# Performance work log

Hardware: AMD Instinct MI355X
Metric: run time of the kernel (lower is better)

Reference implementation:

```python
import jax, jax.numpy as jnp
import numpy as np

N_KNN = 16
BN_EPS = 1e-5


def conv1d(x, w, b):
    # x: [B, Cin, N], w: [Cout, Cin], b: [Cout] (1x1 Conv1d)
    return jnp.einsum('oc,bcn->bon', w, x) + b[None, :, None]


def conv2d(x, w, b):
    # x: [B, Cin, N, K], w: [Cout, Cin], b: [Cout] (1x1 Conv2d)
    return jnp.einsum('oc,bcnk->bonk', w, x) + b[None, :, None, None]


def bn2d(x, gamma, beta, mean, var):
    # eval-mode BatchNorm2d over channel axis 1
    scale = (gamma / jnp.sqrt(var + BN_EPS))[None, :, None, None]
    return (x - mean[None, :, None, None]) * scale + beta[None, :, None, None]


def knn_idx(pos, k):
    # pos: [B, 3, N] -> idx: [B, N, K] of k nearest neighbors (incl. self)
    p = jnp.swapaxes(pos, 1, 2)  # [B, N, 3]
    sq = jnp.sum(p * p, axis=-1)  # [B, N]
    d2 = sq[:, :, None] - 2.0 * jnp.einsum('bnd,bmd->bnm', p, p) + sq[:, None, :]
    _, idx = jax.lax.top_k(-d2, k)
    return idx


def group(x, idx):
    # x: [B, C, N], idx: [B, N, K] -> [B, C, N, K] (grouping_operation)
    return jax.vmap(lambda xb, ib: xb[:, ib])(x, idx)


def setup_inputs() -> dict:
    key = jax.random.key(0)
    B, C_OBJ, C_Q, N, DIM, PH, AM = 4, 512, 512, 4096, 128, 64, 4
    ks = jax.random.split(key, 32)
    r = lambda i, sh, s=0.05: jax.random.normal(ks[i], sh, jnp.float32) * s
    inp = {
        'obj_feature': jax.random.normal(ks[0], (B, C_OBJ, N), jnp.float32),
        'pos': jax.random.normal(ks[1], (B, 3, N), jnp.float32),
        'query_points': jax.random.normal(ks[2], (B, C_Q, N), jnp.float32),
        # linear_start_query / linear_start_obj
        'w_sq': r(3, (DIM, C_Q)), 'b_sq': r(4, (DIM,)),
        'w_so': r(5, (DIM, C_OBJ)), 'b_so': r(6, (DIM,)),
        # key / query / value 1x1 convs
        'w_k': r(7, (DIM, DIM)), 'b_k': r(8, (DIM,)),
        'w_q': r(9, (DIM, DIM)), 'b_q': r(10, (DIM,)),
        'w_v': r(11, (DIM, DIM)), 'b_v': r(12, (DIM,)),
        # pos_mlp: Conv2d(3->PH), BN, ReLU, Conv2d(PH->DIM)
        'w_p1': r(13, (PH, 3)), 'b_p1': r(14, (PH,)),
        'g_bn1': 1.0 + r(15, (PH,)), 'be_bn1': r(16, (PH,)),
        'm_bn1': r(17, (PH,)), 'v_bn1': 1.0 + 0.1 * jax.random.uniform(ks[18], (PH,), jnp.float32),
        'w_p2': r(19, (DIM, PH)), 'b_p2': r(20, (DIM,)),
        # attn_mlp: Conv2d(DIM->DIM*AM), BN, ReLU, Conv2d(DIM*AM->DIM)
        'w_a1': r(21, (DIM * AM, DIM)), 'b_a1': r(22, (DIM * AM,)),
        'g_bn2': 1.0 + r(23, (DIM * AM,)), 'be_bn2': r(24, (DIM * AM,)),
        'm_bn2': r(25, (DIM * AM,)), 'v_bn2': 1.0 + 0.1 * jax.random.uniform(ks[26], (DIM * AM,), jnp.float32),
        # linear_end
        'w_e': r(27, (C_OBJ, DIM)), 'b_e': r(28, (C_OBJ,)),
    }
    return inp


def reference(obj_feature, pos, query_points, w_sq, b_sq, w_so, b_so, w_k, b_k,
              w_q, b_q, w_v, b_v, w_p1, b_p1, g_bn1, be_bn1, m_bn1, v_bn1,
              w_p2, b_p2, w_a1, b_a1, g_bn2, be_bn2, m_bn2, v_bn2, w_e, b_e):
    qf = conv1d(query_points, w_sq, b_sq)          # [B, dim, N]
    f = conv1d(obj_feature, w_so, b_so)            # [B, dim, N]
    idx = knn_idx(jax.lax.stop_gradient(pos), N_KNN)  # [B, N, K]
    key_g = group(conv1d(f, w_k, b_k), idx)        # [B, dim, N, K]
    value = conv1d(f, w_v, b_v)                    # [B, dim, N]
    query = conv1d(qf, w_q, b_q)                   # [B, dim, N]
    qk_rel = query[:, :, :, None] - key_g          # [B, dim, N, K]
    pos_rel = pos[:, :, :, None] - group(pos, idx)  # [B, 3, N, K]
    pe = conv2d(jax.nn.relu(bn2d(conv2d(pos_rel, w_p1, b_p1), g_bn1, be_bn1, m_bn1, v_bn1)), w_p2, b_p2)
    attn = conv2d(jax.nn.relu(bn2d(conv2d(qk_rel + pe, w_a1, b_a1), g_bn2, be_bn2, m_bn2, v_bn2)), w_a2_placeholder := w_p2 * 0 + 0, b_p2 * 0) if False else None
    hidden = jax.nn.relu(bn2d(conv2d(qk_rel + pe, w_a1, b_a1), g_bn2, be_bn2, m_bn2, v_bn2))
    attn = jax.nn.softmax(conv2d(hidden, w_a2, b_a2), axis=-1)  # softmax over K
    v = value[:, :, :, None] + pe                  # [B, dim, N, K]
    agg = jnp.sum(attn * v, axis=-1)               # 'b c i j, b c i j -> b c i'
    return conv1d(agg, w_e, b_e)                   # [B, C_obj, N]

# fix: w_a2/b_a2 are parameters; re-declare reference cleanly to include them

def _setup_extra(inp):
    kk = jax.random.split(jax.random.key(7), 2)
    inp['w_a2'] = jax.random.normal(kk[0], (128, 512), jnp.float32) * 0.05
    inp['b_a2'] = jax.random.normal(kk[1], (128,), jnp.float32) * 0.05
    return inp

_orig_setup = setup_inputs

def setup_inputs():
    return _setup_extra(_orig_setup())


def reference(obj_feature, pos, query_points, w_sq, b_sq, w_so, b_so, w_k, b_k,
              w_q, b_q, w_v, b_v, w_p1, b_p1, g_bn1, be_bn1, m_bn1, v_bn1,
              w_p2, b_p2, w_a1, b_a1, g_bn2, be_bn2, m_bn2, v_bn2, w_a2, b_a2,
              w_e, b_e):
    qf = conv1d(query_points, w_sq, b_sq)
    f = conv1d(obj_feature, w_so, b_so)
    idx = knn_idx(jax.lax.stop_gradient(pos), N_KNN)
    key_g = group(conv1d(f, w_k, b_k), idx)
    value = conv1d(f, w_v, b_v)
    query = conv1d(qf, w_q, b_q)
    qk_rel = query[:, :, :, None] - key_g
    pos_rel = pos[:, :, :, None] - group(pos, idx)
    pe = conv2d(jax.nn.relu(bn2d(conv2d(pos_rel, w_p1, b_p1), g_bn1, be_bn1, m_bn1, v_bn1)), w_p2, b_p2)
    hidden = jax.nn.relu(bn2d(conv2d(qk_rel + pe, w_a1, b_a1), g_bn2, be_bn2, m_bn2, v_bn2))
    attn = jax.nn.softmax(conv2d(hidden, w_a2, b_a2), axis=-1)
    v = value[:, :, :, None] + pe
    agg = jnp.sum(attn * v, axis=-1)
    return conv1d(agg, w_e, b_e)
```

## Files before the change

### kernel.cpp

```cpp
#include <hip/hip_runtime.h>

typedef __bf16 bf16;
typedef __bf16 bf16x8 __attribute__((ext_vector_type(8)));
typedef __bf16 bf16x4 __attribute__((ext_vector_type(4)));
typedef __bf16 bf16x2 __attribute__((ext_vector_type(2)));
typedef float f32x4 __attribute__((ext_vector_type(4)));

#define MFMA16(a,b,c) __builtin_amdgcn_mfma_f32_16x16x32_bf16((a),(b),(c),0,0,0)

#define NPTS 4096
#define CIN 512
#define DIM 128
#define PH 64
#define HID 512

#define OFF_WQS 0u
#define OFF_WKO (128u*1024u)
#define OFF_WVO (256u*1024u)
#define OFF_BQS (384u*1024u)
#define OFF_BKO (385u*1024u)
#define OFF_BVO (386u*1024u)
#define OFF_S1  (387u*1024u)
#define OFF_T1  (388u*1024u)
#define OFF_S2  (389u*1024u)
#define OFF_T2  (391u*1024u)
#define OFF_CW  (400u*1024u)
#define OFF_QT  (1u<<20)
#define OFF_KT  (OFF_QT + (4u<<20))
#define OFF_VT  (OFF_QT + (8u<<20))
#define OFF_IDX (OFF_QT + (12u<<20))
#define WS_NEED (OFF_QT + (13u<<20))

struct P {
  const float* in[31];
  char* ws;
  float* out;
  int ybase;
};

template<int C> __device__ __forceinline__ float rorf(float x){
  return __int_as_float(__builtin_amdgcn_mov_dpp(__float_as_int(x), 0x120|C, 0xF, 0xF, true));
}
__device__ __forceinline__ float red16max(float x){
  x=fmaxf(x,rorf<1>(x)); x=fmaxf(x,rorf<2>(x)); x=fmaxf(x,rorf<4>(x)); x=fmaxf(x,rorf<8>(x)); return x;
}
__device__ __forceinline__ float red16sum(float x){
  x+=rorf<1>(x); x+=rorf<2>(x); x+=rorf<4>(x); x+=rorf<8>(x); return x;
}
template<int C> __device__ __forceinline__ unsigned long long ror64(unsigned long long k){
  unsigned lo = (unsigned)__builtin_amdgcn_mov_dpp((int)(unsigned)k,        0x120|C, 0xF, 0xF, true);
  unsigned hi = (unsigned)__builtin_amdgcn_mov_dpp((int)(unsigned)(k>>32), 0x120|C, 0xF, 0xF, true);
  return ((unsigned long long)hi<<32)|lo;
}

__global__ __launch_bounds__(256) void k_fold(P p) {
  int tid = blockIdx.x*256 + threadIdx.x;
  char* ws = p.ws;
  if (tid < 196608) {
    int m_id = tid >> 16, o = (tid >> 9) & 127, c = tid & 511;
    const float* A  = m_id==0 ? p.in[9] : (m_id==1 ? p.in[7] : p.in[11]);
    const float* Bm = (m_id==0) ? p.in[3] : p.in[5];
    float acc = 0.f;
    #pragma unroll 8
    for (int m=0;m<128;m++) acc += A[o*128+m] * Bm[m*512+c];
    bf16* outw = (bf16*)(ws + (m_id==0?OFF_WQS: m_id==1?OFF_WKO:OFF_WVO));
    outw[o*512+c] = (bf16)acc;
  } else if (tid < 196992) {
    int t = tid - 196608; int m_id = t >> 7, o = t & 127;
    const float* A  = m_id==0 ? p.in[9] : (m_id==1 ? p.in[7] : p.in[11]);
    const float* bb = (m_id==0) ? p.in[4] : p.in[6];
    const float* bs = m_id==0 ? p.in[10] : (m_id==1 ? p.in[8] : p.in[12]);
    float acc = bs[o];
    for (int m=0;m<128;m++) acc += A[o*128+m] * bb[m];
    float* ob = (float*)(ws + (m_id==0?OFF_BQS: m_id==1?OFF_BKO:OFF_BVO));
    ob[o] = acc;
  } else if (tid < 197056) {
    int i = tid - 196992;
    float s = p.in[15][i] * rsqrtf(p.in[18][i] + 1e-5f);
    ((float*)(ws+OFF_S1))[i] = s;
    ((float*)(ws+OFF_T1))[i] = (p.in[14][i] - p.in[17][i])*s + p.in[16][i];
  } else if (tid < 197568) {
    int i = tid - 197056;
    float s = p.in[23][i] * rsqrtf(p.in[26][i] + 1e-5f);
    ((float*)(ws+OFF_S2))[i] = s;
    ((float*)(ws+OFF_T2))[i] = (p.in[22][i] - p.in[25][i])*s + p.in[24][i];
  } else if (tid < 223168) {
    int e0 = (tid - 197568) * 8;
    const float* src; int base;
    if (e0 < 8192)        { src = p.in[19]; base = 0; }
    else if (e0 < 73728)  { src = p.in[21]; base = 8192; }
    else if (e0 < 139264) { src = p.in[29]; base = 73728; }
    else                  { src = p.in[27]; base = 139264; }
    const float* sp = src + (e0 - base);
    f32x4 a = *(const f32x4*)sp, b2 = *(const f32x4*)(sp+4);
    bf16x8 o8;
    o8[0]=(bf16)a[0]; o8[1]=(bf16)a[1]; o8[2]=(bf16)a[2]; o8[3]=(bf16)a[3];
    o8[4]=(bf16)b2[0]; o8[5]=(bf16)b2[1]; o8[6]=(bf16)b2[2]; o8[7]=(bf16)b2[3];
    *(bf16x8*)((bf16*)(ws+OFF_CW) + e0) = o8;
  }
}

__global__ __launch_bounds__(256) void k_knn(P p) {
  int lane = threadIdx.x & 63, w = threadIdx.x >> 6;
  int ig = blockIdx.x*4 + w;
  int b = ig >> 12, n = ig & 4095;
  const float* pb = p.in[1] + b*3*NPTS;
  float qx = pb[n], qy = pb[NPTS+n], qz = pb[2*NPTS+n];
  float sqn = __fadd_rn(__fadd_rn(__fmul_rn(qx,qx), __fmul_rn(qy,qy)), __fmul_rn(qz,qz));
  unsigned u[64];
  #pragma unroll
  for (int t=0;t<64;t++) {
    int j = t*64 + lane;
    float xj=pb[j], yj=pb[NPTS+j], zj=pb[2*NPTS+j];
    float sqj = __fadd_rn(__fadd_rn(__fmul_rn(xj,xj), __fmul_rn(yj,yj)), __fmul_rn(zj,zj));
    float dot = __fadd_rn(__fadd_rn(__fmul_rn(qx,xj), __fmul_rn(qy,yj)), __fmul_rn(qz,zj));
    float d2 = __fadd_rn(__fsub_rn(sqn, __fmul_rn(2.f,dot)), sqj);
    unsigned bb2 = __float_as_uint(d2);
    u[t] = bb2 ^ (((unsigned)((int)bb2 >> 31)) | 0x80000000u);
  }
  int* op = (int*)(p.ws + OFF_IDX) + ig*16;
  int tsel_s = 64; bool mine = false;
  #pragma unroll 1
  for (int r=0;r<16;r++) {
    switch (tsel_s) {
#define CLR(T) case T: u[T] = mine ? 0xFFFFFFFFu : u[T]; break;
      CLR(0) CLR(1) CLR(2) CLR(3) CLR(4) CLR(5) CLR(6) CLR(7)
      CLR(8) CLR(9) CLR(10) CLR(11) CLR(12) CLR(13) CLR(14) CLR(15)
      CLR(16) CLR(17) CLR(18) CLR(19) CLR(20) CLR(21) CLR(22) CLR(23)
      CLR(24) CLR(25) CLR(26) CLR(27) CLR(28) CLR(29) CLR(30) CLR(31)
      CLR(32) CLR(33) CLR(34) CLR(35) CLR(36) CLR(37) CLR(38) CLR(39)
      CLR(40) CLR(41) CLR(42) CLR(43) CLR(44) CLR(45) CLR(46) CLR(47)
      CLR(48) CLR(49) CLR(50) CLR(51) CLR(52) CLR(53) CLR(54) CLR(55)
      CLR(56) CLR(57) CLR(58) CLR(59) CLR(60) CLR(61) CLR(62) CLR(63)
#undef CLR
      default: break;
    }
    unsigned v0=u[0], v1=u[16], v2=u[32], v3=u[48];
    int t0=0, t1=16, t2=32, t3=48;
    #pragma unroll
    for (int i=1;i<16;i++) {
      { bool lt=u[i]    <v0; v0=lt?u[i]   :v0; t0=lt?(i)   :t0; }
      { bool lt=u[16+i] <v1; v1=lt?u[16+i]:v1; t1=lt?(16+i):t1; }
      { bool lt=u[32+i] <v2; v2=lt?u[32+i]:v2; t2=lt?(32+i):t2; }
      { bool lt=u[48+i] <v3; v3=lt?u[48+i]:v3; t3=lt?(48+i):t3; }
    }
    { bool lt=v1<v0; v0=lt?v1:v0; t0=lt?t1:t0; }
    { bool lt=v3<v2; v2=lt?v3:v2; t2=lt?t3:t2; }
    { bool lt=v2<v0; v0=lt?v2:v0; t0=lt?t2:t0; }
    unsigned long long key = ((unsigned long long)v0 << 12) | (unsigned)((t0<<6) | lane);
    { unsigned long long o = ror64<1>(key); if (o<key) key=o; }
    { unsigned long long o = ror64<2>(key); if (o<key) key=o; }
    { unsigned long long o = ror64<4>(key); if (o<key) key=o; }
    { unsigned long long o = ror64<8>(key); if (o<key) key=o; }
    { unsigned long long o = __shfl_xor(key,16); if (o<key) key=o; }
    { unsigned long long o = __shfl_xor(key,32); if (o<key) key=o; }
    unsigned jwin = (unsigned)key & 4095u;
    if (lane==0) op[r] = (int)jwin;
    tsel_s = __builtin_amdgcn_readfirstlane((int)(jwin>>6));
    mine = ((int)(jwin&63)==lane);
  }
}

__global__ __launch_bounds__(256) void k_qkv(P p) {
  int mat = blockIdx.z, b = blockIdx.y, n0 = blockIdx.x*64;
  int tid = threadIdx.x, lane = tid&63, w = tid>>6;
  const float* in = (mat==0 ? p.in[2] : p.in[0]) + b*CIN*NPTS;
  const bf16* W = (const bf16*)(p.ws + (mat==0?OFF_WQS: mat==1?OFF_WKO:OFF_WVO));
  const float* bias = (const float*)(p.ws + (mat==0?OFF_BQS: mat==1?OFF_BKO:OFF_BVO));
  bf16* outT = (bf16*)(p.ws + (mat==0?OFF_QT: mat==1?OFF_KT:OFF_VT)) + (b*NPTS + n0)*DIM;
  __shared__ __align__(16) bf16 Bl[64*40];
  f32x4 acc[8] = {};
  for (int ks=0; ks<16; ks++) {
    int c0 = ks*32;
    {
      int cc = tid>>3, nn0 = (tid&7)*8;
      const float* sp = in + (c0+cc)*NPTS + n0 + nn0;
      f32x4 a = *(const f32x4*)sp, b2 = *(const f32x4*)(sp+4);
      Bl[(nn0+0)*40+cc]=(bf16)a[0];  Bl[(nn0+1)*40+cc]=(bf16)a[1];
      Bl[(nn0+2)*40+cc]=(bf16)a[2];  Bl[(nn0+3)*40+cc]=(bf16)a[3];
      Bl[(nn0+4)*40+cc]=(bf16)b2[0]; Bl[(nn0+5)*40+cc]=(bf16)b2[1];
      Bl[(nn0+6)*40+cc]=(bf16)b2[2]; Bl[(nn0+7)*40+cc]=(bf16)b2[3];
    }
    __syncthreads();
    int ncol = w*16 + (lane&15);
    bf16x8 bfr = *(const bf16x8*)(&Bl[ncol*40 + (lane>>4)*8]);
    #pragma unroll
    for (int ot=0;ot<8;ot++) {
      bf16x8 af = *(const bf16x8*)(W + (ot*16 + (lane&15))*CIN + c0 + (lane>>4)*8);
      acc[ot] = MFMA16(af, bfr, acc[ot]);
    }
    __syncthreads();
  }
  int o0 = (lane>>4)*4;
  int nloc = w*16 + (lane&15);
  #pragma unroll
  for (int ot=0;ot<8;ot++) {
    f32x4 bs = *(const f32x4*)(bias + ot*16 + o0);
    bf16x4 st;
    st[0]=(bf16)(acc[ot][0]+bs[0]); st[1]=(bf16)(acc[ot][1]+bs[1]);
    st[2]=(bf16)(acc[ot][2]+bs[2]); st[3]=(bf16)(acc[ot][3]+bs[3]);
    *(bf16x4*)(outT + nloc*DIM + ot*16 + o0) = st;
  }
}

__global__ __launch_bounds__(512) void k_fused(P p) {
  int bb = p.ybase + blockIdx.y, pt0 = blockIdx.x*8;
  int tid=threadIdx.x, lane=tid&63, w=tid>>6;
  int c = lane&15, g = lane>>4;
  char* ws = p.ws;
  const bf16* qT = (const bf16*)(ws+OFF_QT) + bb*NPTS*DIM;
  const bf16* kT = (const bf16*)(ws+OFF_KT) + bb*NPTS*DIM;
  const bf16* vT = (const bf16*)(ws+OFF_VT) + bb*NPTS*DIM;
  const int* idxg = (const int*)(ws+OFF_IDX) + (bb*NPTS + pt0)*16;
  const bf16* wp2b = (const bf16*)(ws+OFF_CW);
  const bf16* wa1b = wp2b + 8192;
  const bf16* wa2b = wa1b + 65536;
  const bf16* web  = wa2b + 65536;
  const float* s2 = (const float*)(ws+OFF_S2);
  const float* t2 = (const float*)(ws+OFF_T2);
  __shared__ __align__(16) char LB[53248];
  bf16* Xl = (bf16*)LB;
  bf16* HT = (bf16*)(LB + 34816);
  bf16* aggl = (bf16*)(LB + 34816);

  {
    int col = w*16 + c;
    int j = idxg[col] & 4095;
    const float* pb = p.in[1] + bb*3*NPTS;
    int n = pt0 + w;
    float r0 = pb[n]-pb[j], r1 = pb[NPTS+n]-pb[NPTS+j], r2 = pb[2*NPTS+n]-pb[2*NPTS+j];
    const float* wp1 = p.in[13];
    const float* s1 = (const float*)(ws+OFF_S1);
    const float* t1 = (const float*)(ws+OFF_T1);
    #pragma unroll
    for (int i=0;i<16;i+=2) {
      int m = g*16 + i;
      float x0 = wp1[m*3]*r0   + wp1[m*3+1]*r1 + wp1[m*3+2]*r2;
      float x1 = wp1[m*3+3]*r0 + wp1[m*3+4]*r1 + wp1[m*3+5]*r2;
      bf16x2 pk;
      pk[0] = (bf16)fmaxf(0.f, x0*s1[m]   + t1[m]);
      pk[1] = (bf16)fmaxf(0.f, x1*s1[m+1] + t1[m+1]);
      *(bf16x2*)(&HT[col*72 + m]) = pk;
    }
  }
  __syncthreads();

  {
    f32x4 acc[8] = {};
    int crow = w*16 + c;
    #pragma unroll
    for (int ksx=0; ksx<2; ksx++) {
      int m0 = ksx*32 + g*8;
      bf16x8 af = *(const bf16x8*)(wp2b + crow*PH + m0);
      #pragma unroll
      for (int nt=0; nt<8; nt++) {
        int col = nt*16 + c;
        bf16x8 bfr = *(const bf16x8*)(&HT[col*72 + m0]);
        acc[nt] = MFMA16(af, bfr, acc[nt]);
      }
    }
    int c0 = w*16 + g*4;
    f32x4 bp4 = *(const f32x4*)(p.in[20] + c0);
    #pragma unroll
    for (int nt=0; nt<8; nt++) {
      int col = nt*16 + c;
      int j = idxg[col] & 4095;
      int n = pt0 + nt;
      bf16x4 q4 = *(const bf16x4*)(qT + n*DIM + c0);
      bf16x4 k4 = *(const bf16x4*)(kT + j*DIM + c0);
      bf16x4 st;
      #pragma unroll
      for (int r=0;r<4;r++)
        st[r] = (bf16)((float)q4[r] - (float)k4[r] + acc[nt][r] + bp4[r]);
      *(bf16x4*)(&Xl[col*136 + c0]) = st;
    }
  }
  __syncthreads();

  f32x4 S[8] = {};
  for (int ch=0; ch<8; ch++) {
    f32x4 acc1[4] = {};
    int mtw = w & 3, nbase = (w>>2)*4;
    int hrow = ch*64 + mtw*16 + c;
    #pragma unroll
    for (int ksx=0; ksx<4; ksx++) {
      bf16x8 af = *(const bf16x8*)(wa1b + hrow*DIM + ksx*32 + g*8);
      #pragma unroll
      for (int i=0; i<4; i++) {
        int col = (nbase+i)*16 + c;
        bf16x8 bfr = *(const bf16x8*)(&Xl[col*136 + ksx*32 + g*8]);
        acc1[i] = MFMA16(af, bfr, acc1[i]);
      }
    }
    int h0 = ch*64 + mtw*16 + g*4;
    int h0loc = mtw*16 + g*4;
    f32x4 sv = *(const f32x4*)(s2 + h0);
    f32x4 tv = *(const f32x4*)(t2 + h0);
    #pragma unroll
    for (int i=0;i<4;i++) {
      int col = (nbase+i)*16 + c;
      bf16x4 st;
      st[0]=(bf16)fmaxf(0.f, acc1[i][0]*sv[0]+tv[0]);
      st[1]=(bf16)fmaxf(0.f, acc1[i][1]*sv[1]+tv[1]);
      st[2]=(bf16)fmaxf(0.f, acc1[i][2]*sv[2]+tv[2]);
      st[3]=(bf16)fmaxf(0.f, acc1[i][3]*sv[3]+tv[3]);
      *(bf16x4*)(&HT[col*72 + h0loc]) = st;
    }
    __syncthreads();
    int orow = w*16 + c;
    #pragma unroll
    for (int ksx=0; ksx<2; ksx++) {
      bf16x8 af = *(const bf16x8*)(wa2b + orow*HID + ch*64 + ksx*32 + g*8);
      #pragma unroll
      for (int nt=0; nt<8; nt++) {
        int col = nt*16 + c;
        bf16x8 bfr = *(const bf16x8*)(&HT[col*72 + ksx*32 + g*8]);
        S[nt] = MFMA16(af, bfr, S[nt]);
      }
    }
    __syncthreads();
  }

  {
    int c0 = w*16 + g*4;
    #pragma unroll
    for (int nt=0; nt<8; nt++) {
      f32x4 s = S[nt];
      int col = nt*16 + c;
      int j = idxg[col] & 4095;
      int n = pt0 + nt;
      bf16x4 x4 = *(const bf16x4*)(&Xl[col*136 + c0]);
      bf16x4 q4 = *(const bf16x4*)(qT + n*DIM + c0);
      bf16x4 k4 = *(const bf16x4*)(kT + j*DIM + c0);
      bf16x4 v4 = *(const bf16x4*)(vT + n*DIM + c0);
      float agv[4];
      #pragma unroll
      for (int r=0;r<4;r++) {
        float mx = red16max(s[r]);
        float e = __expf(s[r]-mx);
        float sm = red16sum(e);
        float at = e/sm;
        float vpe = (float)v4[r] + (float)x4[r] - (float)q4[r] + (float)k4[r];
        agv[r] = red16sum(at*vpe);
      }
      if (c==0) {
        bf16x4 st; st[0]=(bf16)agv[0]; st[1]=(bf16)agv[1]; st[2]=(bf16)agv[2]; st[3]=(bf16)agv[3];
        *(bf16x4*)(&aggl[nt*136 + c0]) = st;
      }
    }
  }
  __syncthreads();

  {
    const float* be = p.in[28];
    f32x4 acc5[4] = {};
    #pragma unroll
    for (int ksx=0; ksx<4; ksx++) {
      bf16x8 bfr = *(const bf16x8*)(&aggl[c*136 + ksx*32 + g*8]);
      #pragma unroll
      for (int i=0;i<4;i++) {
        int e = (w*4+i)*16 + c;
        bf16x8 af = *(const bf16x8*)(web + e*DIM + ksx*32 + g*8);
        acc5[i] = MFMA16(af, bfr, acc5[i]);
      }
    }
    if (c < 8) {
      int n = pt0 + c;
      #pragma unroll
      for (int i=0;i<4;i++) {
        int e0 = (w*4+i)*16 + g*4;
        f32x4 be4 = *(const f32x4*)(be + e0);
        #pragma unroll
        for (int r=0;r<4;r++)
          p.out[(bb*CIN + e0+r)*NPTS + n] = acc5[i][r] + be4[r];
      }
    }
  }
}

extern "C" void kernel_launch(void* const* d_in, const int* in_sizes, int n_in,
                              void* d_out, int out_size, void* d_ws, size_t ws_size,
                              hipStream_t stream) {
  if (ws_size < WS_NEED || n_in < 31) return;
  P p;
  for (int i=0;i<31;i++) p.in[i] = (const float*)d_in[i];
  p.ws = (char*)d_ws;
  p.out = (float*)d_out;
  p.ybase = 0;
  k_fold<<<872, 256, 0, stream>>>(p);
  k_knn<<<4096, 256, 0, stream>>>(p);
  k_qkv<<<dim3(64, 4, 3), 256, 0, stream>>>(p);
  k_fused<<<dim3(512, 4), 512, 0, stream>>>(p);
}
```

Measured before the change: 444.4 us.

## Use 32x32 MFMA in attention MLP and incremental group-min updates in KNN

The KNN selection now keeps per-group minima across rounds and recomputes only the one 16-entry group whose element was just cleared, instead of rescanning all 64 candidates every round. The fused attention kernel switches its two hidden-layer GEMMs from 16x16x32 to 32x32x16 bf16 MFMA tiles. The wave-to-tile mapping and the softmax/aggregation epilogue are remapped to the new accumulator layout. This cuts redundant compare work in KNN and should raise MFMA efficiency and operand reuse, at the cost of more accumulator registers and a more complex lane mapping.

New measurement: 490.6 us. 1.1x slower.

```diff
diff --git a/kernel.cpp b/kernel.cpp
--- a/kernel.cpp
+++ b/kernel.cpp
@@ -5,8 +5,10 @@
 typedef __bf16 bf16x4 __attribute__((ext_vector_type(4)));
 typedef __bf16 bf16x2 __attribute__((ext_vector_type(2)));
 typedef float f32x4 __attribute__((ext_vector_type(4)));
+typedef float f32x16 __attribute__((ext_vector_type(16)));
 
 #define MFMA16(a,b,c) __builtin_amdgcn_mfma_f32_16x16x32_bf16((a),(b),(c),0,0,0)
+#define MFMA32(a,b,c) __builtin_amdgcn_mfma_f32_32x32x16_bf16((a),(b),(c),0,0,0)
 
 #define NPTS 4096
 #define CIN 512
@@ -118,11 +120,36 @@
     unsigned bb2 = __float_as_uint(d2);
     u[t] = bb2 ^ (((unsigned)((int)bb2 >> 31)) | 0x80000000u);
   }
+  unsigned v0=u[0], v1=u[16], v2=u[32], v3=u[48];
+  int t0=0, t1=16, t2=32, t3=48;
+  #pragma unroll
+  for (int i=1;i<16;i++) {
+    { bool lt=u[i]    <v0; v0=lt?u[i]   :v0; t0=lt?(i)   :t0; }
+    { bool lt=u[16+i] <v1; v1=lt?u[16+i]:v1; t1=lt?(16+i):t1; }
+    { bool lt=u[32+i] <v2; v2=lt?u[32+i]:v2; t2=lt?(32+i):t2; }
+    { bool lt=u[48+i] <v3; v3=lt?u[48+i]:v3; t3=lt?(48+i):t3; }
+  }
   int* op = (int*)(p.ws + OFF_IDX) + ig*16;
-  int tsel_s = 64; bool mine = false;
   #pragma unroll 1
   for (int r=0;r<16;r++) {
-    switch (tsel_s) {
+    unsigned va=v0; int ta=t0;
+    { bool lt=v1<va; va=lt?v1:va; ta=lt?t1:ta; }
+    unsigned vb=v2; int tb=t2;
+    { bool lt=v3<vb; vb=lt?v3:vb; tb=lt?t3:tb; }
+    { bool lt=vb<va; va=lt?vb:va; ta=lt?tb:ta; }
+    unsigned long long key = ((unsigned long long)va << 12) | (unsigned)((ta<<6) | lane);
+    { unsigned long long o = ror64<1>(key); if (o<key) key=o; }
+    { unsigned long long o = ror64<2>(key); if (o<key) key=o; }
+    { unsigned long long o = ror64<4>(key); if (o<key) key=o; }
+    { unsigned long long o = ror64<8>(key); if (o<key) key=o; }
+    { unsigned long long o = __shfl_xor(key,16); if (o<key) key=o; }
+    { unsigned long long o = __shfl_xor(key,32); if (o<key) key=o; }
+    unsigned jwin = (unsigned)key & 4095u;
+    if (lane==0) op[r] = (int)jwin;
+    if (r==15) break;
+    int tsel = __builtin_amdgcn_readfirstlane((int)(jwin>>6));
+    bool mine = ((int)(jwin&63)==lane);
+    switch (tsel) {
 #define CLR(T) case T: u[T] = mine ? 0xFFFFFFFFu : u[T]; break;
       CLR(0) CLR(1) CLR(2) CLR(3) CLR(4) CLR(5) CLR(6) CLR(7)
       CLR(8) CLR(9) CLR(10) CLR(11) CLR(12) CLR(13) CLR(14) CLR(15)
@@ -135,29 +162,20 @@
 #undef CLR
       default: break;
     }
-    unsigned v0=u[0], v1=u[16], v2=u[32], v3=u[48];
-    int t0=0, t1=16, t2=32, t3=48;
-    #pragma unroll
-    for (int i=1;i<16;i++) {
-      { bool lt=u[i]    <v0; v0=lt?u[i]   :v0; t0=lt?(i)   :t0; }
-      { bool lt=u[16+i] <v1; v1=lt?u[16+i]:v1; t1=lt?(16+i):t1; }
-      { bool lt=u[32+i] <v2; v2=lt?u[32+i]:v2; t2=lt?(32+i):t2; }
-      { bool lt=u[48+i] <v3; v3=lt?u[48+i]:v3; t3=lt?(48+i):t3; }
-    }
-    { bool lt=v1<v0; v0=lt?v1:v0; t0=lt?t1:t0; }
-    { bool lt=v3<v2; v2=lt?v3:v2; t2=lt?t3:t2; }
-    { bool lt=v2<v0; v0=lt?v2:v0; t0=lt?t2:t0; }
-    unsigned long long key = ((unsigned long long)v0 << 12) | (unsigned)((t0<<6) | lane);
-    { unsigned long long o = ror64<1>(key); if (o<key) key=o; }
-    { unsigned long long o = ror64<2>(key); if (o<key) key=o; }
-    { unsigned long long o = ror64<4>(key); if (o<key) key=o; }
-    { unsigned long long o = ror64<8>(key); if (o<key) key=o; }
-    { unsigned long long o = __shfl_xor(key,16); if (o<key) key=o; }
-    { unsigned long long o = __shfl_xor(key,32); if (o<key) key=o; }
-    unsigned jwin = (unsigned)key & 4095u;
-    if (lane==0) op[r] = (int)jwin;
-    tsel_s = __builtin_amdgcn_readfirstlane((int)(jwin>>6));
-    mine = ((int)(jwin&63)==lane);
+    switch (tsel >> 4) {
+      case 0: { v0=u[0]; t0=0;
+        #pragma unroll
+        for (int i=1;i<16;i++){ bool lt=u[i]<v0; v0=lt?u[i]:v0; t0=lt?i:t0; } } break;
+      case 1: { v1=u[16]; t1=16;
+        #pragma unroll
+        for (int i=1;i<16;i++){ bool lt=u[16+i]<v1; v1=lt?u[16+i]:v1; t1=lt?(16+i):t1; } } break;
+      case 2: { v2=u[32]; t2=32;
+        #pragma unroll
+        for (int i=1;i<16;i++){ bool lt=u[32+i]<v2; v2=lt?u[32+i]:v2; t2=lt?(32+i):t2; } } break;
+      default: { v3=u[48]; t3=48;
+        #pragma unroll
+        for (int i=1;i<16;i++){ bool lt=u[48+i]<v3; v3=lt?u[48+i]:v3; t3=lt?(48+i):t3; } } break;
+    }
   }
 }
 
@@ -207,6 +225,7 @@
   int bb = p.ybase + blockIdx.y, pt0 = blockIdx.x*8;
   int tid=threadIdx.x, lane=tid&63, w=tid>>6;
   int c = lane&15, g = lane>>4;
+  int l31 = lane & 31, lh = lane >> 5;
   char* ws = p.ws;
   const bf16* qT = (const bf16*)(ws+OFF_QT) + bb*NPTS*DIM;
   const bf16* kT = (const bf16*)(ws+OFF_KT) + bb*NPTS*DIM;
@@ -277,75 +296,72 @@
   }
   __syncthreads();
 
-  f32x4 S[8] = {};
+  f32x16 S0 = {}, S1 = {};
+  int mh = w & 1;
+  int nc = w >> 1;
+  int mo = w & 3;
+  int nc2 = w >> 2;
   for (int ch=0; ch<8; ch++) {
-    f32x4 acc1[4] = {};
-    int mtw = w & 3, nbase = (w>>2)*4;
-    int hrow = ch*64 + mtw*16 + c;
-    #pragma unroll
-    for (int ksx=0; ksx<4; ksx++) {
-      bf16x8 af = *(const bf16x8*)(wa1b + hrow*DIM + ksx*32 + g*8);
-      #pragma unroll
-      for (int i=0; i<4; i++) {
-        int col = (nbase+i)*16 + c;
-        bf16x8 bfr = *(const bf16x8*)(&Xl[col*136 + ksx*32 + g*8]);
-        acc1[i] = MFMA16(af, bfr, acc1[i]);
-      }
-    }
-    int h0 = ch*64 + mtw*16 + g*4;
-    int h0loc = mtw*16 + g*4;
-    f32x4 sv = *(const f32x4*)(s2 + h0);
-    f32x4 tv = *(const f32x4*)(t2 + h0);
-    #pragma unroll
-    for (int i=0;i<4;i++) {
-      int col = (nbase+i)*16 + c;
+    f32x16 acc = {};
+    #pragma unroll
+    for (int kk=0; kk<8; kk++) {
+      bf16x8 af = *(const bf16x8*)(wa1b + (ch*64 + mh*32 + l31)*DIM + kk*16 + lh*8);
+      bf16x8 bfr = *(const bf16x8*)(&Xl[(nc*32 + l31)*136 + kk*16 + lh*8]);
+      acc = MFMA32(af, bfr, acc);
+    }
+    #pragma unroll
+    for (int rq=0; rq<4; rq++) {
+      int hl = mh*32 + rq*8 + lh*4;
+      int hgl = ch*64 + hl;
+      f32x4 sv = *(const f32x4*)(s2 + hgl);
+      f32x4 tv = *(const f32x4*)(t2 + hgl);
       bf16x4 st;
-      st[0]=(bf16)fmaxf(0.f, acc1[i][0]*sv[0]+tv[0]);
-      st[1]=(bf16)fmaxf(0.f, acc1[i][1]*sv[1]+tv[1]);
-      st[2]=(bf16)fmaxf(0.f, acc1[i][2]*sv[2]+tv[2]);
-      st[3]=(bf16)fmaxf(0.f, acc1[i][3]*sv[3]+tv[3]);
-      *(bf16x4*)(&HT[col*72 + h0loc]) = st;
+      st[0]=(bf16)fmaxf(0.f, acc[rq*4+0]*sv[0]+tv[0]);
+      st[1]=(bf16)fmaxf(0.f, acc[rq*4+1]*sv[1]+tv[1]);
+      st[2]=(bf16)fmaxf(0.f, acc[rq*4+2]*sv[2]+tv[2]);
+      st[3]=(bf16)fmaxf(0.f, acc[rq*4+3]*sv[3]+tv[3]);
+      *(bf16x4*)(&HT[(nc*32 + l31)*72 + hl]) = st;
     }
     __syncthreads();
-    int orow = w*16 + c;
-    #pragma unroll
-    for (int ksx=0; ksx<2; ksx++) {
-      bf16x8 af = *(const bf16x8*)(wa2b + orow*HID + ch*64 + ksx*32 + g*8);
-      #pragma unroll
-      for (int nt=0; nt<8; nt++) {
-        int col = nt*16 + c;
-        bf16x8 bfr = *(const bf16x8*)(&HT[col*72 + ksx*32 + g*8]);
-        S[nt] = MFMA16(af, bfr, S[nt]);
-      }
+    #pragma unroll
+    for (int kk=0; kk<4; kk++) {
+      bf16x8 af = *(const bf16x8*)(wa2b + (mo*32 + l31)*HID + ch*64 + kk*16 + lh*8);
+      bf16x8 b0 = *(const bf16x8*)(&HT[(nc2*64 + l31)*72 + kk*16 + lh*8]);
+      bf16x8 b1 = *(const bf16x8*)(&HT[(nc2*64 + 32 + l31)*72 + kk*16 + lh*8]);
+      S0 = MFMA32(af, b0, S0);
+      S1 = MFMA32(af, b1, S1);
     }
     __syncthreads();
   }
 
-  {
-    int c0 = w*16 + g*4;
-    #pragma unroll
-    for (int nt=0; nt<8; nt++) {
-      f32x4 s = S[nt];
-      int col = nt*16 + c;
-      int j = idxg[col] & 4095;
-      int n = pt0 + nt;
-      bf16x4 x4 = *(const bf16x4*)(&Xl[col*136 + c0]);
-      bf16x4 q4 = *(const bf16x4*)(qT + n*DIM + c0);
-      bf16x4 k4 = *(const bf16x4*)(kT + j*DIM + c0);
-      bf16x4 v4 = *(const bf16x4*)(vT + n*DIM + c0);
+  #pragma unroll
+  for (int t=0; t<2; t++) {
+    f32x16 Sv = t ? S1 : S0;
+    int ptl = nc2*4 + t*2 + ((lane>>4)&1);
+    int colg = ptl*16 + c;
+    int j = idxg[colg] & 4095;
+    int n = pt0 + ptl;
+    #pragma unroll
+    for (int rq=0; rq<4; rq++) {
+      int chb = mo*32 + rq*8 + lh*4;
+      bf16x4 x4 = *(const bf16x4*)(&Xl[colg*136 + chb]);
+      bf16x4 q4 = *(const bf16x4*)(qT + n*DIM + chb);
+      bf16x4 k4 = *(const bf16x4*)(kT + j*DIM + chb);
+      bf16x4 v4 = *(const bf16x4*)(vT + n*DIM + chb);
       float agv[4];
       #pragma unroll
-      for (int r=0;r<4;r++) {
-        float mx = red16max(s[r]);
-        float e = __expf(s[r]-mx);
+      for (int r2=0; r2<4; r2++) {
+        float s = Sv[rq*4+r2];
+        float mx = red16max(s);
+        float e = __expf(s-mx);
         float sm = red16sum(e);
         float at = e/sm;
-        float vpe = (float)v4[r] + (float)x4[r] - (float)q4[r] + (float)k4[r];
-        agv[r] = red16sum(at*vpe);
+        float vpe = (float)v4[r2] + (float)x4[r2] - (float)q4[r2] + (float)k4[r2];
+        agv[r2] = red16sum(at*vpe);
       }
       if (c==0) {
         bf16x4 st; st[0]=(bf16)agv[0]; st[1]=(bf16)agv[1]; st[2]=(bf16)agv[2]; st[3]=(bf16)agv[3];
-        *(bf16x4*)(&aggl[nt*136 + c0]) = st;
+        *(bf16x4*)(&aggl[ptl*136 + chb]) = st;
       }
     }
   }
```

## Merge KNN and QKV kernels; rescan only the affected quarter in top-k

Applied to the files above, without the earlier changes.

Merges the QKV projection GEMM and the KNN search into one launch. The first 768 blocks do the projections and the remaining 4096 do KNN, so the two independent workloads can overlap on the GPU and one launch is saved. In KNN top-k selection, per-quarter minima are kept across rounds, and only the 16-element quarter holding the removed winner is rescanned instead of all 64 registers. The trade-offs are that the merged kernel takes the larger register and LDS footprint of both paths, and the switch on the quarter index may add branch overhead.

After: 404.1 us. 1.1x faster.

```diff
diff --git a/kernel.cpp b/kernel.cpp
--- a/kernel.cpp
+++ b/kernel.cpp
@@ -100,9 +100,52 @@
   }
 }
 
-__global__ __launch_bounds__(256) void k_knn(P p) {
+__global__ __launch_bounds__(256) void k_knnqkv(P p) {
+  if (blockIdx.x < 768) {
+    int qb = blockIdx.x;
+    int mat = qb >> 8, b = (qb >> 6) & 3, n0 = (qb & 63) * 64;
+    int tid = threadIdx.x, lane = tid&63, w = tid>>6;
+    const float* in = (mat==0 ? p.in[2] : p.in[0]) + b*CIN*NPTS;
+    const bf16* W = (const bf16*)(p.ws + (mat==0?OFF_WQS: mat==1?OFF_WKO:OFF_WVO));
+    const float* bias = (const float*)(p.ws + (mat==0?OFF_BQS: mat==1?OFF_BKO:OFF_BVO));
+    bf16* outT = (bf16*)(p.ws + (mat==0?OFF_QT: mat==1?OFF_KT:OFF_VT)) + (b*NPTS + n0)*DIM;
+    __shared__ __align__(16) bf16 Bl[64*40];
+    f32x4 acc[8] = {};
+    for (int ks=0; ks<16; ks++) {
+      int c0 = ks*32;
+      {
+        int cc = tid>>3, nn0 = (tid&7)*8;
+        const float* sp = in + (c0+cc)*NPTS + n0 + nn0;
+        f32x4 a = *(const f32x4*)sp, b2 = *(const f32x4*)(sp+4);
+        Bl[(nn0+0)*40+cc]=(bf16)a[0];  Bl[(nn0+1)*40+cc]=(bf16)a[1];
+        Bl[(nn0+2)*40+cc]=(bf16)a[2];  Bl[(nn0+3)*40+cc]=(bf16)a[3];
+        Bl[(nn0+4)*40+cc]=(bf16)b2[0]; Bl[(nn0+5)*40+cc]=(bf16)b2[1];
+        Bl[(nn0+6)*40+cc]=(bf16)b2[2]; Bl[(nn0+7)*40+cc]=(bf16)b2[3];
+      }
+      __syncthreads();
+      int ncol = w*16 + (lane&15);
+      bf16x8 bfr = *(const bf16x8*)(&Bl[ncol*40 + (lane>>4)*8]);
+      #pragma unroll
+      for (int ot=0;ot<8;ot++) {
+        bf16x8 af = *(const bf16x8*)(W + (ot*16 + (lane&15))*CIN + c0 + (lane>>4)*8);
+        acc[ot] = MFMA16(af, bfr, acc[ot]);
+      }
+      __syncthreads();
+    }
+    int o0 = (lane>>4)*4;
+    int nloc = w*16 + (lane&15);
+    #pragma unroll
+    for (int ot=0;ot<8;ot++) {
+      f32x4 bs = *(const f32x4*)(bias + ot*16 + o0);
+      bf16x4 st;
+      st[0]=(bf16)(acc[ot][0]+bs[0]); st[1]=(bf16)(acc[ot][1]+bs[1]);
+      st[2]=(bf16)(acc[ot][2]+bs[2]); st[3]=(bf16)(acc[ot][3]+bs[3]);
+      *(bf16x4*)(outT + nloc*DIM + ot*16 + o0) = st;
+    }
+    return;
+  }
   int lane = threadIdx.x & 63, w = threadIdx.x >> 6;
-  int ig = blockIdx.x*4 + w;
+  int ig = (blockIdx.x - 768)*4 + w;
   int b = ig >> 12, n = ig & 4095;
   const float* pb = p.in[1] + b*3*NPTS;
   float qx = pb[n], qy = pb[NPTS+n], qz = pb[2*NPTS+n];
@@ -118,11 +161,36 @@
     unsigned bb2 = __float_as_uint(d2);
     u[t] = bb2 ^ (((unsigned)((int)bb2 >> 31)) | 0x80000000u);
   }
+  unsigned v0=u[0], v1=u[16], v2=u[32], v3=u[48];
+  int t0=0, t1=16, t2=32, t3=48;
+  #pragma unroll
+  for (int i=1;i<16;i++) {
+    { bool lt=u[i]    <v0; v0=lt?u[i]   :v0; t0=lt?(i)   :t0; }
+    { bool lt=u[16+i] <v1; v1=lt?u[16+i]:v1; t1=lt?(16+i):t1; }
+    { bool lt=u[32+i] <v2; v2=lt?u[32+i]:v2; t2=lt?(32+i):t2; }
+    { bool lt=u[48+i] <v3; v3=lt?u[48+i]:v3; t3=lt?(48+i):t3; }
+  }
   int* op = (int*)(p.ws + OFF_IDX) + ig*16;
-  int tsel_s = 64; bool mine = false;
   #pragma unroll 1
   for (int r=0;r<16;r++) {
-    switch (tsel_s) {
+    unsigned va=v0; int ta=t0;
+    { bool lt=v1<va; va=lt?v1:va; ta=lt?t1:ta; }
+    unsigned vb=v2; int tb=t2;
+    { bool lt=v3<vb; vb=lt?v3:vb; tb=lt?t3:tb; }
+    { bool lt=vb<va; va=lt?vb:va; ta=lt?tb:ta; }
+    unsigned long long key = ((unsigned long long)va << 12) | (unsigned)((ta<<6) | lane);
+    { unsigned long long o = ror64<1>(key); if (o<key) key=o; }
+    { unsigned long long o = ror64<2>(key); if (o<key) key=o; }
+    { unsigned long long o = ror64<4>(key); if (o<key) key=o; }
+    { unsigned long long o = ror64<8>(key); if (o<key) key=o; }
+    { unsigned long long o = __shfl_xor(key,16); if (o<key) key=o; }
+    { unsigned long long o = __shfl_xor(key,32); if (o<key) key=o; }
+    unsigned jwin = (unsigned)key & 4095u;
+    if (lane==0) op[r] = (int)jwin;
+    if (r==15) break;
+    int tsel = __builtin_amdgcn_readfirstlane((int)(jwin>>6));
+    bool mine = ((int)(jwin&63)==lane);
+    switch (tsel) {
 #define CLR(T) case T: u[T] = mine ? 0xFFFFFFFFu : u[T]; break;
       CLR(0) CLR(1) CLR(2) CLR(3) CLR(4) CLR(5) CLR(6) CLR(7)
       CLR(8) CLR(9) CLR(10) CLR(11) CLR(12) CLR(13) CLR(14) CLR(15)
@@ -135,71 +203,20 @@
 #undef CLR
       default: break;
     }
-    unsigned v0=u[0], v1=u[16], v2=u[32], v3=u[48];
-    int t0=0, t1=16, t2=32, t3=48;
-    #pragma unroll
-    for (int i=1;i<16;i++) {
-      { bool lt=u[i]    <v0; v0=lt?u[i]   :v0; t0=lt?(i)   :t0; }
-      { bool lt=u[16+i] <v1; v1=lt?u[16+i]:v1; t1=lt?(16+i):t1; }
-      { bool lt=u[32+i] <v2; v2=lt?u[32+i]:v2; t2=lt?(32+i):t2; }
-      { bool lt=u[48+i] <v3; v3=lt?u[48+i]:v3; t3=lt?(48+i):t3; }
-    }
-    { bool lt=v1<v0; v0=lt?v1:v0; t0=lt?t1:t0; }
-    { bool lt=v3<v2; v2=lt?v3:v2; t2=lt?t3:t2; }
-    { bool lt=v2<v0; v0=lt?v2:v0; t0=lt?t2:t0; }
-    unsigned long long key = ((unsigned long long)v0 << 12) | (unsigned)((t0<<6) | lane);
-    { unsigned long long o = ror64<1>(key); if (o<key) key=o; }
-    { unsigned long long o = ror64<2>(key); if (o<key) key=o; }
-    { unsigned long long o = ror64<4>(key); if (o<key) key=o; }
-    { unsigned long long o = ror64<8>(key); if (o<key) key=o; }
-    { unsigned long long o = __shfl_xor(key,16); if (o<key) key=o; }
-    { unsigned long long o = __shfl_xor(key,32); if (o<key) key=o; }
-    unsigned jwin = (unsigned)key & 4095u;
-    if (lane==0) op[r] = (int)jwin;
-    tsel_s = __builtin_amdgcn_readfirstlane((int)(jwin>>6));
-    mine = ((int)(jwin&63)==lane);
-  }
-}
-
-__global__ __launch_bounds__(256) void k_qkv(P p) {
-  int mat = blockIdx.z, b = blockIdx.y, n0 = blockIdx.x*64;
-  int tid = threadIdx.x, lane = tid&63, w = tid>>6;
-  const float* in = (mat==0 ? p.in[2] : p.in[0]) + b*CIN*NPTS;
-  const bf16* W = (const bf16*)(p.ws + (mat==0?OFF_WQS: mat==1?OFF_WKO:OFF_WVO));
-  const float* bias = (const float*)(p.ws + (mat==0?OFF_BQS: mat==1?OFF_BKO:OFF_BVO));
-  bf16* outT = (bf16*)(p.ws + (mat==0?OFF_QT: mat==1?OFF_KT:OFF_VT)) + (b*NPTS + n0)*DIM;
-  __shared__ __align__(16) bf16 Bl[64*40];
-  f32x4 acc[8] = {};
-  for (int ks=0; ks<16; ks++) {
-    int c0 = ks*32;
-    {
-      int cc = tid>>3, nn0 = (tid&7)*8;
-      const float* sp = in + (c0+cc)*NPTS + n0 + nn0;
-      f32x4 a = *(const f32x4*)sp, b2 = *(const f32x4*)(sp+4);
-      Bl[(nn0+0)*40+cc]=(bf16)a[0];  Bl[(nn0+1)*40+cc]=(bf16)a[1];
-      Bl[(nn0+2)*40+cc]=(bf16)a[2];  Bl[(nn0+3)*40+cc]=(bf16)a[3];
-      Bl[(nn0+4)*40+cc]=(bf16)b2[0]; Bl[(nn0+5)*40+cc]=(bf16)b2[1];
-      Bl[(nn0+6)*40+cc]=(bf16)b2[2]; Bl[(nn0+7)*40+cc]=(bf16)b2[3];
-    }
-    __syncthreads();
-    int ncol = w*16 + (lane&15);
-    bf16x8 bfr = *(const bf16x8*)(&Bl[ncol*40 + (lane>>4)*8]);
-    #pragma unroll
-    for (int ot=0;ot<8;ot++) {
-      bf16x8 af = *(const bf16x8*)(W + (ot*16 + (lane&15))*CIN + c0 + (lane>>4)*8);
-      acc[ot] = MFMA16(af, bfr, acc[ot]);
-    }
-    __syncthreads();
-  }
-  int o0 = (lane>>4)*4;
-  int nloc = w*16 + (lane&15);
-  #pragma unroll
-  for (int ot=0;ot<8;ot++) {
-    f32x4 bs = *(const f32x4*)(bias + ot*16 + o0);
-    bf16x4 st;
-    st[0]=(bf16)(acc[ot][0]+bs[0]); st[1]=(bf16)(acc[ot][1]+bs[1]);
-    st[2]=(bf16)(acc[ot][2]+bs[2]); st[3]=(bf16)(acc[ot][3]+bs[3]);
-    *(bf16x4*)(outT + nloc*DIM + ot*16 + o0) = st;
+    switch (tsel >> 4) {
+      case 0: { v0=u[0]; t0=0;
+        #pragma unroll
+        for (int i=1;i<16;i++){ bool lt=u[i]<v0; v0=lt?u[i]:v0; t0=lt?i:t0; } } break;
+      case 1: { v1=u[16]; t1=16;
+        #pragma unroll
+        for (int i=1;i<16;i++){ bool lt=u[16+i]<v1; v1=lt?u[16+i]:v1; t1=lt?(16+i):t1; } } break;
+      case 2: { v2=u[32]; t2=32;
+        #pragma unroll
+        for (int i=1;i<16;i++){ bool lt=u[32+i]<v2; v2=lt?u[32+i]:v2; t2=lt?(32+i):t2; } } break;
+      default: { v3=u[48]; t3=48;
+        #pragma unroll
+        for (int i=1;i<16;i++){ bool lt=u[48+i]<v3; v3=lt?u[48+i]:v3; t3=lt?(48+i):t3; } } break;
+    }
   }
 }
 
@@ -388,7 +405,6 @@
   p.out = (float*)d_out;
   p.ybase = 0;
   k_fold<<<872, 256, 0, stream>>>(p);
-  k_knn<<<4096, 256, 0, stream>>>(p);
-  k_qkv<<<dim3(64, 4, 3), 256, 0, stream>>>(p);
+  k_knnqkv<<<768 + 4096, 256, 0, stream>>>(p);
   k_fused<<<dim3(512, 4), 512, 0, stream>>>(p);
 }
```
